# Kernel tuning notes

Measured on AMD Instinct MI355X. Metric: run time of the kernel, lower is better.

Reference implementation:

```python
import jax, jax.numpy as jnp
import numpy as np

N_EDGES = 1_000_000
N_NODES = 500_000
N_TRIS = 600_000
C = 64


def setup_inputs() -> dict:
    key = jax.random.key(0)
    k1, k2, k3, k4, k5, k6 = jax.random.split(key, 6)
    x = jax.random.normal(k1, (N_EDGES, C), dtype=jnp.float32)
    # B1: each edge has tail (-1) and head (+1) node
    edge_nodes = jax.random.randint(k2, (N_EDGES, 2), 0, N_NODES, dtype=jnp.int64)
    # B2: each triangle touches 3 edges with signs (+1, -1, +1)
    tri_edges = jax.random.randint(k3, (N_TRIS, 3), 0, N_EDGES, dtype=jnp.int64)
    scale = 1.0 / np.sqrt(C)
    w0 = jax.random.normal(k4, (C, C), dtype=jnp.float32) * scale
    w1 = jax.random.normal(k5, (C, C), dtype=jnp.float32) * scale
    w2 = jax.random.normal(k6, (C, C), dtype=jnp.float32) * scale
    return {"x": x, "edge_nodes": edge_nodes, "tri_edges": tri_edges,
            "w0": w0, "w1": w1, "w2": w2}


def reference(x, edge_nodes, tri_edges, w0, w1, w2):
    tail, head = edge_nodes[:, 0], edge_nodes[:, 1]
    e0, e1, e2 = tri_edges[:, 0], tri_edges[:, 1], tri_edges[:, 2]

    y = jnp.zeros((N_NODES, C), x.dtype).at[tail].add(-x).at[head].add(x)
    # B1^T y: gather back to edges with signs
    z3 = (y[head] - y[tail]) @ w0

    # z1 = B2 B2^T x @ w2  (up-Laplacian term)
    # B2^T x: signed gather onto triangles, shape [T, C]
    w = x[e0] - x[e1] + x[e2]
    # B2 w: signed scatter back to edges
    z1e = jnp.zeros((N_EDGES, C), x.dtype).at[e0].add(w).at[e1].add(-w).at[e2].add(w)
    z1 = z1e @ w2

    # z2 = x @ w1 (identity term)
    z2 = x @ w1

    # sum aggregation + tanh update
    return jnp.tanh(z1 + z2 + z3)
```

## Files before the change

kernel.cpp:

```cpp
#include <hip/hip_runtime.h>
#include <hip/hip_bf16.h>

#define N_EDGES 1000000
#define N_NODES 500000
#define N_TRIS  600000

typedef __attribute__((ext_vector_type(8))) short bf16x8;
typedef __attribute__((ext_vector_type(4))) float f32x4;

__device__ __forceinline__ float fast_tanh(float z) {
    z = fminf(fmaxf(z, -15.0f), 15.0f);
    float e = __expf(2.0f * z);
    return (e - 1.0f) / (e + 1.0f);
}

__global__ __launch_bounds__(256) void k_scatter_y(
    const float* __restrict__ x, const int* __restrict__ en, float* __restrict__ y)
{
    int idx = blockIdx.x * 256 + threadIdx.x;
    int e = idx >> 6, c = idx & 63;
    float v = x[idx];
    int tail = en[2 * e];
    int head = en[2 * e + 1];
    unsafeAtomicAdd(&y[(size_t)tail * 64 + c], -v);
    unsafeAtomicAdd(&y[(size_t)head * 64 + c],  v);
}

__global__ __launch_bounds__(256) void k_scatter_z1e(
    const float* __restrict__ x, const int* __restrict__ te, float* __restrict__ z1e)
{
    int idx = blockIdx.x * 256 + threadIdx.x;
    int t = idx >> 6, c = idx & 63;
    int e0 = te[3 * t], e1 = te[3 * t + 1], e2 = te[3 * t + 2];
    float w = x[(size_t)e0 * 64 + c] - x[(size_t)e1 * 64 + c] + x[(size_t)e2 * 64 + c];
    unsafeAtomicAdd(&z1e[(size_t)e0 * 64 + c],  w);
    unsafeAtomicAdd(&z1e[(size_t)e1 * 64 + c], -w);
    unsafeAtomicAdd(&z1e[(size_t)e2 * 64 + c],  w);
}

#define AST 48
#define WST 200

__global__ __launch_bounds__(256) void k_final(
    const float* __restrict__ x, const int* __restrict__ en,
    const float* __restrict__ y, float* __restrict__ zio,
    const float* __restrict__ w0, const float* __restrict__ w1,
    const float* __restrict__ w2)
{
    __shared__ __hip_bfloat16 WThi[64 * WST];
    __shared__ __hip_bfloat16 WTlo[64 * WST];
    __shared__ __hip_bfloat16 Ahi[64 * AST];
    __shared__ __hip_bfloat16 Alo[64 * AST];
    __shared__ int nidx[128];

    const int t = threadIdx.x;
    const int ebase = blockIdx.x * 64;

    for (int idx = t; idx < 12288; idx += 256) {
        int k = idx >> 6;
        int n = idx & 63;
        const float* Wsrc = (k < 64) ? w2 : ((k < 128) ? w1 : w0);
        float v = Wsrc[(k & 63) * 64 + n];
        __hip_bfloat16 h = __float2bfloat16(v);
        WThi[n * WST + k] = h;
        WTlo[n * WST + k] = __float2bfloat16(v - __bfloat162float(h));
    }
    if (t < 128) {
        int e = ebase + (t & 63);
        nidx[t] = en[2 * e + (t >> 6)];
    }

    const int r    = t >> 2;
    const int q    = t & 3;
    const int lane = t & 63;
    const int w    = t >> 6;
    const int mrow = lane & 15;
    const int quad = lane >> 4;

    f32x4 acc[4] = {{0,0,0,0},{0,0,0,0},{0,0,0,0},{0,0,0,0}};

    for (int ch = 0; ch < 6; ++ch) {
        const int h = ch & 1;
        float4 v0, v1;
        if (ch < 2) {
            const float4* s = (const float4*)(zio + (size_t)(ebase + r) * 64 + h * 32 + q * 8);
            v0 = s[0]; v1 = s[1];
        } else if (ch < 4) {
            const float4* s = (const float4*)(x + (size_t)(ebase + r) * 64 + h * 32 + q * 8);
            v0 = s[0]; v1 = s[1];
        } else {
            const float4* sh = (const float4*)(y + (size_t)nidx[64 + r] * 64 + h * 32 + q * 8);
            const float4* st = (const float4*)(y + (size_t)nidx[r] * 64 + h * 32 + q * 8);
            float4 a0 = sh[0], a1 = sh[1], b0 = st[0], b1 = st[1];
            v0.x = a0.x - b0.x; v0.y = a0.y - b0.y; v0.z = a0.z - b0.z; v0.w = a0.w - b0.w;
            v1.x = a1.x - b1.x; v1.y = a1.y - b1.y; v1.z = a1.z - b1.z; v1.w = a1.w - b1.w;
        }
        __syncthreads();
        {
            float vv[8] = {v0.x, v0.y, v0.z, v0.w, v1.x, v1.y, v1.z, v1.w};
            #pragma unroll
            for (int j = 0; j < 8; ++j) {
                __hip_bfloat16 hi = __float2bfloat16(vv[j]);
                Ahi[r * AST + q * 8 + j] = hi;
                Alo[r * AST + q * 8 + j] = __float2bfloat16(vv[j] - __bfloat162float(hi));
            }
        }
        __syncthreads();

        const bf16x8 ah = *(const bf16x8*)&Ahi[(w * 16 + mrow) * AST + quad * 8];
        const bf16x8 al = *(const bf16x8*)&Alo[(w * 16 + mrow) * AST + quad * 8];
        #pragma unroll
        for (int nt = 0; nt < 4; ++nt) {
            const bf16x8 bh = *(const bf16x8*)&WThi[(nt * 16 + mrow) * WST + ch * 32 + quad * 8];
            const bf16x8 bl = *(const bf16x8*)&WTlo[(nt * 16 + mrow) * WST + ch * 32 + quad * 8];
            acc[nt] = __builtin_amdgcn_mfma_f32_16x16x32_bf16(ah, bh, acc[nt], 0, 0, 0);
            acc[nt] = __builtin_amdgcn_mfma_f32_16x16x32_bf16(al, bh, acc[nt], 0, 0, 0);
            acc[nt] = __builtin_amdgcn_mfma_f32_16x16x32_bf16(ah, bl, acc[nt], 0, 0, 0);
        }
    }

    #pragma unroll
    for (int nt = 0; nt < 4; ++nt) {
        #pragma unroll
        for (int i = 0; i < 4; ++i) {
            int e = ebase + w * 16 + quad * 4 + i;
            int c = nt * 16 + mrow;
            zio[(size_t)e * 64 + c] = fast_tanh(acc[nt][i]);
        }
    }
}

extern "C" void kernel_launch(void* const* d_in, const int* in_sizes, int n_in,
                              void* d_out, int out_size, void* d_ws, size_t ws_size,
                              hipStream_t stream) {
    const float* x  = (const float*)d_in[0];
    const int*   en = (const int*)d_in[1];
    const int*   te = (const int*)d_in[2];
    const float* w0 = (const float*)d_in[3];
    const float* w1 = (const float*)d_in[4];
    const float* w2 = (const float*)d_in[5];
    float* out = (float*)d_out;
    float* y   = (float*)d_ws;

    hipMemsetAsync(y,   0, (size_t)N_NODES * 64 * sizeof(float), stream);
    hipMemsetAsync(out, 0, (size_t)N_EDGES * 64 * sizeof(float), stream);

    k_scatter_y  <<<(N_EDGES * 64) / 256, 256, 0, stream>>>(x, en, y);
    k_scatter_z1e<<<(N_TRIS  * 64) / 256, 256, 0, stream>>>(x, te, out);
    k_final      <<<N_EDGES / 64,        256, 0, stream>>>(x, en, y, out, w0, w1, w2);
}
```

Measured before the change: 1.597 ms.

## Use packed float2 atomics in scatters and register-resident weights with double-buffered A tiles

The scatter kernels now have each thread handle two channels and use packed 2-wide float atomic adds, which halves the number of atomic instructions and threads. The final GEMM kernel keeps split-bf16 weight fragments in registers instead of shared memory. It double-buffers the A tile in LDS with one barrier per chunk, prefetches the next chunk's global loads, and transposes the wave-to-tile mapping. These changes cut LDS footprint, sync count and atomic traffic, at the cost of higher register pressure under launch_bounds(256,3) and a reliance on the packed atomic builtin being available.

```diff
diff --git a/kernel.cpp b/kernel.cpp
--- a/kernel.cpp
+++ b/kernel.cpp
@@ -7,6 +7,7 @@
 
 typedef __attribute__((ext_vector_type(8))) short bf16x8;
 typedef __attribute__((ext_vector_type(4))) float f32x4;
+typedef __attribute__((ext_vector_type(2))) float f32x2;
 
 __device__ __forceinline__ float fast_tanh(float z) {
     z = fminf(fmaxf(z, -15.0f), 15.0f);
@@ -14,118 +15,164 @@
     return (e - 1.0f) / (e + 1.0f);
 }
 
+__device__ __forceinline__ void atomic_pk_add(float* p, f32x2 v) {
+#if __has_builtin(__builtin_amdgcn_flat_atomic_fadd_v2f32)
+    __builtin_amdgcn_flat_atomic_fadd_v2f32((f32x2*)p, v);
+#else
+    unsafeAtomicAdd(p, v.x);
+    unsafeAtomicAdd(p + 1, v.y);
+#endif
+}
+
+__device__ __forceinline__ short bf16_hi_bits(float v, float& hv) {
+    __hip_bfloat16 h = __float2bfloat16(v);
+    hv = __bfloat162float(h);
+    short s; __builtin_memcpy(&s, &h, 2); return s;
+}
+__device__ __forceinline__ short bf16_bits(float v) {
+    __hip_bfloat16 h = __float2bfloat16(v);
+    short s; __builtin_memcpy(&s, &h, 2); return s;
+}
+
 __global__ __launch_bounds__(256) void k_scatter_y(
     const float* __restrict__ x, const int* __restrict__ en, float* __restrict__ y)
 {
     int idx = blockIdx.x * 256 + threadIdx.x;
-    int e = idx >> 6, c = idx & 63;
-    float v = x[idx];
+    int e = idx >> 5, c2 = idx & 31;
+    f32x2 v = ((const f32x2*)x)[(size_t)e * 32 + c2];
     int tail = en[2 * e];
     int head = en[2 * e + 1];
-    unsafeAtomicAdd(&y[(size_t)tail * 64 + c], -v);
-    unsafeAtomicAdd(&y[(size_t)head * 64 + c],  v);
+    atomic_pk_add(&y[(size_t)tail * 64 + 2 * c2], -v);
+    atomic_pk_add(&y[(size_t)head * 64 + 2 * c2],  v);
 }
 
 __global__ __launch_bounds__(256) void k_scatter_z1e(
     const float* __restrict__ x, const int* __restrict__ te, float* __restrict__ z1e)
 {
     int idx = blockIdx.x * 256 + threadIdx.x;
-    int t = idx >> 6, c = idx & 63;
+    int t = idx >> 5, c2 = idx & 31;
     int e0 = te[3 * t], e1 = te[3 * t + 1], e2 = te[3 * t + 2];
-    float w = x[(size_t)e0 * 64 + c] - x[(size_t)e1 * 64 + c] + x[(size_t)e2 * 64 + c];
-    unsafeAtomicAdd(&z1e[(size_t)e0 * 64 + c],  w);
-    unsafeAtomicAdd(&z1e[(size_t)e1 * 64 + c], -w);
-    unsafeAtomicAdd(&z1e[(size_t)e2 * 64 + c],  w);
+    const f32x2* x2 = (const f32x2*)x;
+    f32x2 w = x2[(size_t)e0 * 32 + c2] - x2[(size_t)e1 * 32 + c2] + x2[(size_t)e2 * 32 + c2];
+    atomic_pk_add(&z1e[(size_t)e0 * 64 + 2 * c2],  w);
+    atomic_pk_add(&z1e[(size_t)e1 * 64 + 2 * c2], -w);
+    atomic_pk_add(&z1e[(size_t)e2 * 64 + 2 * c2],  w);
 }
 
-#define AST 48
-#define WST 200
+#define AST 40
 
-__global__ __launch_bounds__(256) void k_final(
+__global__ __launch_bounds__(256, 3) void k_final(
     const float* __restrict__ x, const int* __restrict__ en,
     const float* __restrict__ y, float* __restrict__ zio,
     const float* __restrict__ w0, const float* __restrict__ w1,
     const float* __restrict__ w2)
 {
-    __shared__ __hip_bfloat16 WThi[64 * WST];
-    __shared__ __hip_bfloat16 WTlo[64 * WST];
-    __shared__ __hip_bfloat16 Ahi[64 * AST];
-    __shared__ __hip_bfloat16 Alo[64 * AST];
+    __shared__ short Ahi[2][64 * AST];
+    __shared__ short Alo[2][64 * AST];
     __shared__ int nidx[128];
 
-    const int t = threadIdx.x;
+    const int t     = threadIdx.x;
     const int ebase = blockIdx.x * 64;
+    const int lane  = t & 63;
+    const int w     = t >> 6;
+    const int mrow  = lane & 15;
+    const int quad  = lane >> 4;
 
-    for (int idx = t; idx < 12288; idx += 256) {
-        int k = idx >> 6;
-        int n = idx & 63;
-        const float* Wsrc = (k < 64) ? w2 : ((k < 128) ? w1 : w0);
-        float v = Wsrc[(k & 63) * 64 + n];
-        __hip_bfloat16 h = __float2bfloat16(v);
-        WThi[n * WST + k] = h;
-        WTlo[n * WST + k] = __float2bfloat16(v - __bfloat162float(h));
+    bf16x8 Bhi[6], Blo[6];
+    {
+        const int n = w * 16 + mrow;
+        #pragma unroll
+        for (int ch = 0; ch < 6; ++ch) {
+            const float* Wsrc = (ch < 2) ? w2 : ((ch < 4) ? w1 : w0);
+            const int kb = (ch & 1) * 32 + quad * 8;
+            bf16x8 bh, bl;
+            #pragma unroll
+            for (int j = 0; j < 8; ++j) {
+                float v = Wsrc[(kb + j) * 64 + n];
+                float hv;
+                bh[j] = bf16_hi_bits(v, hv);
+                bl[j] = bf16_bits(v - hv);
+            }
+            Bhi[ch] = bh; Blo[ch] = bl;
+        }
     }
-    if (t < 128) {
-        int e = ebase + (t & 63);
-        nidx[t] = en[2 * e + (t >> 6)];
-    }
+
+    if (t < 128) nidx[t] = en[2 * (ebase + (t & 63)) + (t >> 6)];
 
     const int r    = t >> 2;
     const int q    = t & 3;
-    const int lane = t & 63;
-    const int w    = t >> 6;
-    const int mrow = lane & 15;
-    const int quad = lane >> 4;
+    const int koff = q * 8;
 
     f32x4 acc[4] = {{0,0,0,0},{0,0,0,0},{0,0,0,0},{0,0,0,0}};
 
+    float4 pa0, pa1, pb0, pb1;
+
+    {
+        const float4* s = (const float4*)(zio + (size_t)(ebase + r) * 64 + koff);
+        pa0 = s[0]; pa1 = s[1];
+    }
+
+    #pragma unroll
     for (int ch = 0; ch < 6; ++ch) {
-        const int h = ch & 1;
-        float4 v0, v1;
-        if (ch < 2) {
-            const float4* s = (const float4*)(zio + (size_t)(ebase + r) * 64 + h * 32 + q * 8);
-            v0 = s[0]; v1 = s[1];
-        } else if (ch < 4) {
-            const float4* s = (const float4*)(x + (size_t)(ebase + r) * 64 + h * 32 + q * 8);
-            v0 = s[0]; v1 = s[1];
-        } else {
-            const float4* sh = (const float4*)(y + (size_t)nidx[64 + r] * 64 + h * 32 + q * 8);
-            const float4* st = (const float4*)(y + (size_t)nidx[r] * 64 + h * 32 + q * 8);
-            float4 a0 = sh[0], a1 = sh[1], b0 = st[0], b1 = st[1];
-            v0.x = a0.x - b0.x; v0.y = a0.y - b0.y; v0.z = a0.z - b0.z; v0.w = a0.w - b0.w;
-            v1.x = a1.x - b1.x; v1.y = a1.y - b1.y; v1.z = a1.z - b1.z; v1.w = a1.w - b1.w;
-        }
-        __syncthreads();
+        const int b = ch & 1;
+
         {
-            float vv[8] = {v0.x, v0.y, v0.z, v0.w, v1.x, v1.y, v1.z, v1.w};
+            float vv[8];
+            if (ch >= 4) {
+                vv[0] = pa0.x - pb0.x; vv[1] = pa0.y - pb0.y;
+                vv[2] = pa0.z - pb0.z; vv[3] = pa0.w - pb0.w;
+                vv[4] = pa1.x - pb1.x; vv[5] = pa1.y - pb1.y;
+                vv[6] = pa1.z - pb1.z; vv[7] = pa1.w - pb1.w;
+            } else {
+                vv[0] = pa0.x; vv[1] = pa0.y; vv[2] = pa0.z; vv[3] = pa0.w;
+                vv[4] = pa1.x; vv[5] = pa1.y; vv[6] = pa1.z; vv[7] = pa1.w;
+            }
+            bf16x8 hi, lo;
             #pragma unroll
             for (int j = 0; j < 8; ++j) {
-                __hip_bfloat16 hi = __float2bfloat16(vv[j]);
-                Ahi[r * AST + q * 8 + j] = hi;
-                Alo[r * AST + q * 8 + j] = __float2bfloat16(vv[j] - __bfloat162float(hi));
+                float hv;
+                hi[j] = bf16_hi_bits(vv[j], hv);
+                lo[j] = bf16_bits(vv[j] - hv);
+            }
+            *(bf16x8*)&Ahi[b][r * AST + koff] = hi;
+            *(bf16x8*)&Alo[b][r * AST + koff] = lo;
+        }
+
+        if (ch < 5) {
+            const int nc  = ch + 1;
+            const int off = (nc & 1) * 32 + koff;
+            if (nc < 2) {
+                const float4* s = (const float4*)(zio + (size_t)(ebase + r) * 64 + off);
+                pa0 = s[0]; pa1 = s[1];
+            } else if (nc < 4) {
+                const float4* s = (const float4*)(x + (size_t)(ebase + r) * 64 + off);
+                pa0 = s[0]; pa1 = s[1];
+            } else {
+                const float4* sh = (const float4*)(y + (size_t)nidx[64 + r] * 64 + off);
+                const float4* st = (const float4*)(y + (size_t)nidx[r]      * 64 + off);
+                pa0 = sh[0]; pa1 = sh[1]; pb0 = st[0]; pb1 = st[1];
             }
         }
+
         __syncthreads();
 
-        const bf16x8 ah = *(const bf16x8*)&Ahi[(w * 16 + mrow) * AST + quad * 8];
-        const bf16x8 al = *(const bf16x8*)&Alo[(w * 16 + mrow) * AST + quad * 8];
         #pragma unroll
-        for (int nt = 0; nt < 4; ++nt) {
-            const bf16x8 bh = *(const bf16x8*)&WThi[(nt * 16 + mrow) * WST + ch * 32 + quad * 8];
-            const bf16x8 bl = *(const bf16x8*)&WTlo[(nt * 16 + mrow) * WST + ch * 32 + quad * 8];
-            acc[nt] = __builtin_amdgcn_mfma_f32_16x16x32_bf16(ah, bh, acc[nt], 0, 0, 0);
-            acc[nt] = __builtin_amdgcn_mfma_f32_16x16x32_bf16(al, bh, acc[nt], 0, 0, 0);
-            acc[nt] = __builtin_amdgcn_mfma_f32_16x16x32_bf16(ah, bl, acc[nt], 0, 0, 0);
+        for (int mt = 0; mt < 4; ++mt) {
+            const bf16x8 ah = *(const bf16x8*)&Ahi[b][(mt * 16 + mrow) * AST + quad * 8];
+            const bf16x8 al = *(const bf16x8*)&Alo[b][(mt * 16 + mrow) * AST + quad * 8];
+            acc[mt] = __builtin_amdgcn_mfma_f32_16x16x32_bf16(ah, Bhi[ch], acc[mt], 0, 0, 0);
+            acc[mt] = __builtin_amdgcn_mfma_f32_16x16x32_bf16(al, Bhi[ch], acc[mt], 0, 0, 0);
+            acc[mt] = __builtin_amdgcn_mfma_f32_16x16x32_bf16(ah, Blo[ch], acc[mt], 0, 0, 0);
         }
     }
 
     #pragma unroll
-    for (int nt = 0; nt < 4; ++nt) {
+    for (int mt = 0; mt < 4; ++mt) {
         #pragma unroll
         for (int i = 0; i < 4; ++i) {
-            int e = ebase + w * 16 + quad * 4 + i;
-            int c = nt * 16 + mrow;
-            zio[(size_t)e * 64 + c] = fast_tanh(acc[nt][i]);
+            int e = ebase + mt * 16 + quad * 4 + i;
+            int c = w * 16 + mrow;
+            zio[(size_t)e * 64 + c] = fast_tanh(acc[mt][i]);
         }
     }
 }
@@ -145,7 +192,7 @@
     hipMemsetAsync(y,   0, (size_t)N_NODES * 64 * sizeof(float), stream);
     hipMemsetAsync(out, 0, (size_t)N_EDGES * 64 * sizeof(float), stream);
 
-    k_scatter_y  <<<(N_EDGES * 64) / 256, 256, 0, stream>>>(x, en, y);
-    k_scatter_z1e<<<(N_TRIS  * 64) / 256, 256, 0, stream>>>(x, te, out);
-    k_final      <<<N_EDGES / 64,        256, 0, stream>>>(x, en, y, out, w0, w1, w2);
+    k_scatter_y  <<<(N_EDGES * 32) / 256, 256, 0, stream>>>(x, en, y);
+    k_scatter_z1e<<<(N_TRIS  * 32) / 256, 256, 0, stream>>>(x, te, out);
+    k_final      <<<N_EDGES / 64,         256, 0, stream>>>(x, en, y, out, w0, w1, w2);
 }
```

Measured after the change: 2.128 ms. 33.3% more time.
